# Kernel optimization log

Hardware: AMD Instinct MI355X
Metric: run time of the kernel (lower is better)

Reference implementation:

```python
import jax, jax.numpy as jnp
import numpy as np

N, L, H, K = 1024, 128, 768, 5  # sentences, padded seq len, bert hidden, top_iw


def _make_spans(nt, rng):
    # K non-overlapping spans inside token positions [1, nt]; invalid -> (-1, -2)
    n = nt.shape[0]
    step = np.maximum(nt // K, 1)
    j = np.arange(K)
    starts = 1 + j[None, :] * step[:, None]
    width = np.maximum(step[:, None] // 2 - 1, 0)
    ends = np.minimum(starts + width, nt[:, None])
    valid = starts <= nt[:, None]
    valid &= ~(rng.random(n) < 0.1)[:, None]
    starts = np.where(valid, starts, -1)
    ends = np.where(valid, ends, -2)
    return starts.astype(np.int32), ends.astype(np.int32)


def setup_inputs() -> dict:
    key = jax.random.key(0)
    k1, k2 = jax.random.split(key)
    rng = np.random.default_rng(0)
    rev_nt = rng.integers(4, L - 1, N).astype(np.int32)   # tokens per sentence (excl. [CLS]/[SEP])
    rep_nt = rng.integers(4, L - 1, N).astype(np.int32)
    rs, re = _make_spans(rev_nt, rng)
    ps, pe = _make_spans(rep_nt, rng)
    return {
        "review_feat": jax.random.normal(k1, (N, L, H), dtype=jnp.float32),
        "reply_feat": jax.random.normal(k2, (N, L, H), dtype=jnp.float32),
        "review_num_tokens": jnp.asarray(rev_nt),
        "reply_num_tokens": jnp.asarray(rep_nt),
        "review_span_start": jnp.asarray(rs),
        "review_span_end": jnp.asarray(re),
        "reply_span_start": jnp.asarray(ps),
        "reply_span_end": jnp.asarray(pe),
    }


def _pool(feat, num_tokens, span_start, span_end):
    # feat: [N, L, H]; sentence mean over tokens 1..num_tokens (inclusive),
    # probing-topic mean over union of non-overlapping [start, end] spans.
    p = jnp.arange(feat.shape[1])                                  # [L]
    sm = ((p[None, :] >= 1) & (p[None, :] <= num_tokens[:, None])).astype(feat.dtype)  # [N, L]
    sent_mean = jnp.einsum("nl,nlh->nh", sm, feat) / sm.sum(1, keepdims=True)
    in_span = (p[None, None, :] >= span_start[:, :, None]) & (p[None, None, :] <= span_end[:, :, None])
    span_mask = in_span.any(1)                                     # [N, L] (spans non-overlapping)
    has_span = span_mask.any(1)                                    # [N]
    spm = span_mask.astype(feat.dtype)
    cnt = jnp.maximum(spm.sum(1, keepdims=True), 1.0)
    pt_mean = jnp.einsum("nl,nlh->nh", spm, feat) / cnt
    pt = jnp.where(has_span[:, None], pt_mean, sent_mean)
    return pt, sent_mean


def reference(review_feat, reply_feat, review_num_tokens, reply_num_tokens,
              review_span_start, review_span_end, reply_span_start, reply_span_end):
    review_pt, review_sent = _pool(review_feat, review_num_tokens, review_span_start, review_span_end)
    reply_pt, reply_sent = _pool(reply_feat, reply_num_tokens, reply_span_start, reply_span_end)
    return review_pt, review_sent, reply_pt, reply_sent
```

## Files before the change

### kernel.cpp

```cpp
#include <hip/hip_runtime.h>

#define N_SENT 1024
#define LSEQ   128
#define HDIM   768
#define KSPAN  5
#define TPB    192
#define UNROLL 8

__global__ __launch_bounds__(TPB) void bert_pool_kernel(
    const float* __restrict__ review_feat,
    const float* __restrict__ reply_feat,
    const int*   __restrict__ review_nt,
    const int*   __restrict__ reply_nt,
    const int*   __restrict__ review_ss,
    const int*   __restrict__ review_se,
    const int*   __restrict__ reply_ss,
    const int*   __restrict__ reply_se,
    float*       __restrict__ out)
{
    const int n   = blockIdx.x;
    const int tid = threadIdx.x;
    const bool is_reply = (blockIdx.y != 0);

    const float* feat = is_reply ? reply_feat : review_feat;
    const int*   ntp  = is_reply ? reply_nt   : review_nt;
    const int*   ssp  = is_reply ? reply_ss   : review_ss;
    const int*   sep  = is_reply ? reply_se   : review_se;
    float* out_pt   = out + (is_reply ? 2 : 0) * (size_t)N_SENT * HDIM;
    float* out_sent = out + (is_reply ? 3 : 1) * (size_t)N_SENT * HDIM;

    const int nt = ntp[n];

    int s[KSPAN], e[KSPAN];
    int l_lo = 1, l_hi = nt;
#pragma unroll
    for (int k = 0; k < KSPAN; ++k) {
        s[k] = ssp[(size_t)n * KSPAN + k];
        e[k] = sep[(size_t)n * KSPAN + k];
        if (s[k] <= e[k]) {
            if (s[k] < l_lo) l_lo = s[k];
            if (e[k] > l_hi) l_hi = e[k];
        }
    }
    if (l_lo < 0) l_lo = 0;
    if (l_hi > LSEQ - 1) l_hi = LSEQ - 1;

    const float4* frow = (const float4*)(feat + (size_t)n * LSEQ * HDIM);

    float sx = 0.f, sy = 0.f, sz = 0.f, sw = 0.f;
    float px = 0.f, py = 0.f, pz = 0.f, pw = 0.f;
    float span_cnt = 0.f;

    for (int l0 = l_lo; l0 <= l_hi; l0 += UNROLL) {
        float4 v[UNROLL];
        float  ms[UNROLL], mp[UNROLL];
#pragma unroll
        for (int i = 0; i < UNROLL; ++i) {
            const int l    = l0 + i;
            const bool live = (l <= l_hi);
            const int  lc   = live ? l : l_hi;
            v[i] = frow[(size_t)lc * (HDIM / 4) + tid];
            ms[i] = (live && l >= 1 && l <= nt) ? 1.0f : 0.0f;
            bool insp = false;
#pragma unroll
            for (int k = 0; k < KSPAN; ++k)
                insp = insp || ((l >= s[k]) && (l <= e[k]));
            mp[i] = (live && insp) ? 1.0f : 0.0f;
        }
#pragma unroll
        for (int i = 0; i < UNROLL; ++i) {
            sx = fmaf(v[i].x, ms[i], sx);
            sy = fmaf(v[i].y, ms[i], sy);
            sz = fmaf(v[i].z, ms[i], sz);
            sw = fmaf(v[i].w, ms[i], sw);
            px = fmaf(v[i].x, mp[i], px);
            py = fmaf(v[i].y, mp[i], py);
            pz = fmaf(v[i].z, mp[i], pz);
            pw = fmaf(v[i].w, mp[i], pw);
            span_cnt += mp[i];
        }
    }

    const float sent_cnt = (float)(nt < LSEQ - 1 ? nt : LSEQ - 1);
    const float inv_s = 1.0f / sent_cnt;
    const float smx = sx * inv_s, smy = sy * inv_s, smz = sz * inv_s, smw = sw * inv_s;

    const bool has_span = (span_cnt > 0.5f);
    const float inv_p = 1.0f / fmaxf(span_cnt, 1.0f);
    const float ptx = has_span ? px * inv_p : smx;
    const float pty = has_span ? py * inv_p : smy;
    const float ptz = has_span ? pz * inv_p : smz;
    const float ptw = has_span ? pw * inv_p : smw;

    float4* opt = (float4*)(out_pt   + (size_t)n * HDIM);
    float4* osn = (float4*)(out_sent + (size_t)n * HDIM);
    opt[tid] = make_float4(ptx, pty, ptz, ptw);
    osn[tid] = make_float4(smx, smy, smz, smw);
}

extern "C" void kernel_launch(void* const* d_in, const int* in_sizes, int n_in,
                              void* d_out, int out_size, void* d_ws, size_t ws_size,
                              hipStream_t stream) {
    const float* review_feat = (const float*)d_in[0];
    const float* reply_feat  = (const float*)d_in[1];
    const int*   review_nt   = (const int*)d_in[2];
    const int*   reply_nt    = (const int*)d_in[3];
    const int*   review_ss   = (const int*)d_in[4];
    const int*   review_se   = (const int*)d_in[5];
    const int*   reply_ss    = (const int*)d_in[6];
    const int*   reply_se    = (const int*)d_in[7];
    float* out = (float*)d_out;

    dim3 grid(N_SENT, 2);
    bert_pool_kernel<<<grid, TPB, 0, stream>>>(
        review_feat, reply_feat, review_nt, reply_nt,
        review_ss, review_se, reply_ss, reply_se, out);
}
```

Baseline: 101.2 us.

## Split sequence reduction into chunked partial sums with a second combine kernel

Splits each sentence's token reduction across four 32-token chunks in separate blocks, writing partial sentence and span sums plus span counts to workspace. A second kernel adds the partials and computes the means and the fallback. This adds parallelism and memory-level concurrency for a load that is bound by memory bandwidth, at the cost of an extra kernel launch and about 50 MB of workspace traffic. It also relies on phase 2 reading only chunks that phase 1 wrote.

New measurement: 107.6 us. +6.3%, slower.

```diff
diff --git a/kernel.cpp b/kernel.cpp
--- a/kernel.cpp
+++ b/kernel.cpp
@@ -6,33 +6,17 @@
 #define KSPAN  5
 #define TPB    192
 #define UNROLL 8
+#define CHUNK  32
+#define NCHUNK (LSEQ / CHUNK)
+#define SLOT_FLOATS (2 * HDIM)
+#define CNT_OFFSET  ((size_t)2 * N_SENT * NCHUNK * SLOT_FLOATS)
 
-__global__ __launch_bounds__(TPB) void bert_pool_kernel(
-    const float* __restrict__ review_feat,
-    const float* __restrict__ reply_feat,
-    const int*   __restrict__ review_nt,
-    const int*   __restrict__ reply_nt,
-    const int*   __restrict__ review_ss,
-    const int*   __restrict__ review_se,
-    const int*   __restrict__ reply_ss,
-    const int*   __restrict__ reply_se,
-    float*       __restrict__ out)
+__device__ __forceinline__ void load_meta(
+    const int* ntp, const int* ssp, const int* sep, int n,
+    int& nt, int* s, int* e, int& l_lo, int& l_hi)
 {
-    const int n   = blockIdx.x;
-    const int tid = threadIdx.x;
-    const bool is_reply = (blockIdx.y != 0);
-
-    const float* feat = is_reply ? reply_feat : review_feat;
-    const int*   ntp  = is_reply ? reply_nt   : review_nt;
-    const int*   ssp  = is_reply ? reply_ss   : review_ss;
-    const int*   sep  = is_reply ? reply_se   : review_se;
-    float* out_pt   = out + (is_reply ? 2 : 0) * (size_t)N_SENT * HDIM;
-    float* out_sent = out + (is_reply ? 3 : 1) * (size_t)N_SENT * HDIM;
-
-    const int nt = ntp[n];
-
-    int s[KSPAN], e[KSPAN];
-    int l_lo = 1, l_hi = nt;
+    nt = ntp[n];
+    l_lo = 1; l_hi = nt;
 #pragma unroll
     for (int k = 0; k < KSPAN; ++k) {
         s[k] = ssp[(size_t)n * KSPAN + k];
@@ -44,6 +28,36 @@
     }
     if (l_lo < 0) l_lo = 0;
     if (l_hi > LSEQ - 1) l_hi = LSEQ - 1;
+}
+
+__global__ __launch_bounds__(TPB) void pool_phase1(
+    const float* __restrict__ review_feat,
+    const float* __restrict__ reply_feat,
+    const int*   __restrict__ review_nt,
+    const int*   __restrict__ reply_nt,
+    const int*   __restrict__ review_ss,
+    const int*   __restrict__ review_se,
+    const int*   __restrict__ reply_ss,
+    const int*   __restrict__ reply_se,
+    float*       __restrict__ ws)
+{
+    const int n   = blockIdx.x;
+    const int tid = threadIdx.x;
+    const bool is_reply = (blockIdx.y != 0);
+    const int c   = blockIdx.z;
+
+    const float* feat = is_reply ? reply_feat : review_feat;
+    const int*   ntp  = is_reply ? reply_nt   : review_nt;
+    const int*   ssp  = is_reply ? reply_ss   : review_ss;
+    const int*   sep  = is_reply ? reply_se   : review_se;
+
+    int nt, s[KSPAN], e[KSPAN], l_lo, l_hi;
+    load_meta(ntp, ssp, sep, n, nt, s, e, l_lo, l_hi);
+
+    const int c0 = c * CHUNK;
+    const int r0 = l_lo > c0 ? l_lo : c0;
+    const int r1 = l_hi < c0 + CHUNK - 1 ? l_hi : c0 + CHUNK - 1;
+    if (r0 > r1) return;
 
     const float4* frow = (const float4*)(feat + (size_t)n * LSEQ * HDIM);
 
@@ -51,14 +65,14 @@
     float px = 0.f, py = 0.f, pz = 0.f, pw = 0.f;
     float span_cnt = 0.f;
 
-    for (int l0 = l_lo; l0 <= l_hi; l0 += UNROLL) {
+    for (int l0 = r0; l0 <= r1; l0 += UNROLL) {
         float4 v[UNROLL];
         float  ms[UNROLL], mp[UNROLL];
 #pragma unroll
         for (int i = 0; i < UNROLL; ++i) {
-            const int l    = l0 + i;
-            const bool live = (l <= l_hi);
-            const int  lc   = live ? l : l_hi;
+            const int  l    = l0 + i;
+            const bool live = (l <= r1);
+            const int  lc   = live ? l : r1;
             v[i] = frow[(size_t)lc * (HDIM / 4) + tid];
             ms[i] = (live && l >= 1 && l <= nt) ? 1.0f : 0.0f;
             bool insp = false;
@@ -81,17 +95,68 @@
         }
     }
 
+    const int item = (is_reply ? N_SENT : 0) + n;
+    const size_t slot = (size_t)item * NCHUNK + c;
+    float4* psent = (float4*)(ws + slot * SLOT_FLOATS);
+    float4* pspan = psent + HDIM / 4;
+    psent[tid] = make_float4(sx, sy, sz, sw);
+    pspan[tid] = make_float4(px, py, pz, pw);
+    if (tid == 0) ws[CNT_OFFSET + slot] = span_cnt;
+}
+
+__global__ __launch_bounds__(TPB) void pool_phase2(
+    const int* __restrict__ review_nt,
+    const int* __restrict__ reply_nt,
+    const int* __restrict__ review_ss,
+    const int* __restrict__ review_se,
+    const int* __restrict__ reply_ss,
+    const int* __restrict__ reply_se,
+    const float* __restrict__ ws,
+    float*       __restrict__ out)
+{
+    const int n   = blockIdx.x;
+    const int tid = threadIdx.x;
+    const bool is_reply = (blockIdx.y != 0);
+
+    const int* ntp = is_reply ? reply_nt : review_nt;
+    const int* ssp = is_reply ? reply_ss : review_ss;
+    const int* sep = is_reply ? reply_se : review_se;
+
+    int nt, s[KSPAN], e[KSPAN], l_lo, l_hi;
+    load_meta(ntp, ssp, sep, n, nt, s, e, l_lo, l_hi);
+
+    const int c_lo = l_lo / CHUNK;
+    const int c_hi = l_hi / CHUNK;
+    const int item = (is_reply ? N_SENT : 0) + n;
+
+    float sx = 0.f, sy = 0.f, sz = 0.f, sw = 0.f;
+    float px = 0.f, py = 0.f, pz = 0.f, pw = 0.f;
+    float span_cnt = 0.f;
+
+    for (int c = c_lo; c <= c_hi; ++c) {
+        const size_t slot = (size_t)item * NCHUNK + c;
+        const float4* psent = (const float4*)(ws + slot * SLOT_FLOATS);
+        const float4* pspan = psent + HDIM / 4;
+        float4 a = psent[tid];
+        float4 b = pspan[tid];
+        sx += a.x; sy += a.y; sz += a.z; sw += a.w;
+        px += b.x; py += b.y; pz += b.z; pw += b.w;
+        span_cnt += ws[CNT_OFFSET + slot];
+    }
+
     const float sent_cnt = (float)(nt < LSEQ - 1 ? nt : LSEQ - 1);
     const float inv_s = 1.0f / sent_cnt;
     const float smx = sx * inv_s, smy = sy * inv_s, smz = sz * inv_s, smw = sw * inv_s;
 
-    const bool has_span = (span_cnt > 0.5f);
+    const bool  has_span = (span_cnt > 0.5f);
     const float inv_p = 1.0f / fmaxf(span_cnt, 1.0f);
     const float ptx = has_span ? px * inv_p : smx;
     const float pty = has_span ? py * inv_p : smy;
     const float ptz = has_span ? pz * inv_p : smz;
     const float ptw = has_span ? pw * inv_p : smw;
 
+    float* out_pt   = out + (is_reply ? 2 : 0) * (size_t)N_SENT * HDIM;
+    float* out_sent = out + (is_reply ? 3 : 1) * (size_t)N_SENT * HDIM;
     float4* opt = (float4*)(out_pt   + (size_t)n * HDIM);
     float4* osn = (float4*)(out_sent + (size_t)n * HDIM);
     opt[tid] = make_float4(ptx, pty, ptz, ptw);
@@ -110,9 +175,14 @@
     const int*   reply_ss    = (const int*)d_in[6];
     const int*   reply_se    = (const int*)d_in[7];
     float* out = (float*)d_out;
+    float* ws  = (float*)d_ws;
 
-    dim3 grid(N_SENT, 2);
-    bert_pool_kernel<<<grid, TPB, 0, stream>>>(
+    dim3 g1(N_SENT, 2, NCHUNK);
+    pool_phase1<<<g1, TPB, 0, stream>>>(
         review_feat, reply_feat, review_nt, reply_nt,
-        review_ss, review_se, reply_ss, reply_se, out);
+        review_ss, review_se, reply_ss, reply_se, ws);
+
+    dim3 g2(N_SENT, 2);
+    pool_phase2<<<g2, TPB, 0, stream>>>(
+        review_nt, reply_nt, review_ss, review_se, reply_ss, reply_se, ws, out);
 }
```
